# Optimization experiments

Measured on AMD Instinct MI355X. Metric: run time of the kernel, lower is better.

Reference implementation:

```python
import jax, jax.numpy as jnp
import numpy as np

EPS = 1e-5

def _layernorm(x, g, b):
    m = jnp.mean(x, axis=-1, keepdims=True)
    v = jnp.mean((x - m) ** 2, axis=-1, keepdims=True)
    return (x - m) * jax.lax.rsqrt(v + EPS) * g + b

def setup_inputs() -> dict:
    key = jax.random.key(0)
    ks = jax.random.split(key, 8)
    B, S, E, F = 32, 4096, 8, 512
    return {
        "x": jax.random.normal(ks[0], (B, S, E), dtype=jnp.float32),
        "W_in_attn": jax.random.normal(ks[1], (E, E), dtype=jnp.float32) * (1.0 / np.sqrt(E)),
        "theta_attn": jax.random.normal(ks[2], (E,), dtype=jnp.float32),
        "W_out": jax.random.normal(ks[3], (E, E), dtype=jnp.float32) * (1.0 / np.sqrt(E)),
        "theta_ffn": jax.random.normal(ks[4], (E,), dtype=jnp.float32),
        "W1": jax.random.normal(ks[5], (F, E), dtype=jnp.float32) * (1.0 / np.sqrt(E)),
        "b1": jnp.zeros((F,), dtype=jnp.float32),
        "W2": jax.random.normal(ks[6], (E, F), dtype=jnp.float32) * (1.0 / np.sqrt(F)),
        "b2": jnp.zeros((E,), dtype=jnp.float32),
        "ln1_g": jnp.ones((E,), dtype=jnp.float32),
        "ln1_b": jnp.zeros((E,), dtype=jnp.float32),
        "ln2_g": jnp.ones((E,), dtype=jnp.float32),
        "ln2_b": jnpp_zeros((E,)) if False else jnp.zeros((E,), dtype=jnp.float32),
    }

def reference(x, W_in_attn, theta_attn, W_out, theta_ffn, W1, b1, W2, b2,
              ln1_g, ln1_b, ln2_g, ln2_b):
    # --- quantum attention ---
    # per-wire circuit: RX(v_i) then trainable RX(theta_i) on |0>; <Z> = cos(v_i + theta_i)
    tv = jnp.einsum('bse,fe->bsf', x, W_in_attn)          # [B,S,8] input_proj (no bias)
    q_attn = jnp.cos(tv + theta_attn)                      # batched state-vector sim, closed form
    attn_out = jnp.einsum('bsf,ef->bse', q_attn, W_out)    # out_proj (no bias)
    # gate_residual=False, dropout inactive (eval)
    h = _layernorm(x + attn_out, ln1_g, ln1_b)
    # --- quantum FFN ---
    # per-wire circuit: RX(h_i) then trainable RY(theta_i); <Z> = cos(h_i) * cos(theta_i)
    q_ffn = jnp.cos(h) * jnp.cos(theta_ffn)               # [B,S,8]
    mid = jnp.einsum('bse,fe->bsf', q_ffn, W1) + b1        # linear1 -> [B,S,512]
    ffn_out = jnp.einsum('bsf,ef->bsf' if False else 'bsf,ef->bse', jax.nn.relu(mid), W2) + b2
    return _layernorm(h + ffn_out, ln2_g, ln2_b)
```

## Files before the change

### kernel.cpp

```cpp
#include <hip/hip_runtime.h>


typedef __attribute__((ext_vector_type(8)))  short short8;
typedef __attribute__((ext_vector_type(4)))  float f32x4;
typedef __attribute__((ext_vector_type(16))) float f32x16;
typedef __attribute__((ext_vector_type(4)))  int   int4v;

constexpr int E   = 8;
constexpr int F   = 512;
constexpr int TPB = 256;

static __device__ __forceinline__ int cvt_pk_bf16(float lo, float hi) {
    int r;
    asm("v_cvt_pk_bf16_f32 %0, %1, %2" : "=v"(r) : "v"(lo), "v"(hi));
    return r;
}

static __device__ __forceinline__ int hilo_bf16(float v) {
    unsigned u = __builtin_bit_cast(unsigned, v);
    float fh = __builtin_bit_cast(float, u & 0xFFFF0000u);
    return cvt_pk_bf16(fh, v - fh);
}

__global__ __launch_bounds__(512, 4) void qtb_kernel(
    const float* __restrict__ x,
    const float* __restrict__ Win,
    const float* __restrict__ th_attn,
    const float* __restrict__ Wout,
    const float* __restrict__ th_ffn,
    const float* __restrict__ W1,
    const float* __restrict__ b1,
    const float* __restrict__ W2,
    const float* __restrict__ b2,
    const float* __restrict__ g1, const float* __restrict__ bb1,
    const float* __restrict__ g2, const float* __restrict__ bb2,
    float* __restrict__ out, int ntok)
{
    __shared__ short8 wab[1024];
    __shared__ short8 w2p[512];
    __shared__ short8 attnA[64];
    __shared__ short8 woutp[64];

    const int tid  = threadIdx.x;
    const int lane = tid & 63;
    const int wv   = tid >> 6;
    const int t32  = lane & 31;
    const int hi   = lane >> 5;
    const int e8   = t32 & 7;

    {
        const f32x4* w1v = reinterpret_cast<const f32x4*>(W1 + tid * 8);
        f32x4 a = w1v[0], b = w1v[1];
        int4v rw1 = { cvt_pk_bf16(a[0], a[1]), cvt_pk_bf16(a[2], a[3]),
                      cvt_pk_bf16(b[0], b[1]), cvt_pk_bf16(b[2], b[3]) };
        wab[((tid >> 5) << 6) + (tid & 31)] = __builtin_bit_cast(short8, rw1);
        int4v rb1 = { hilo_bf16(b1[tid]), 0, 0, 0 };
        wab[((tid >> 5) << 6) + 32 + (tid & 31)] = __builtin_bit_cast(short8, rb1);
        const int se = tid & 7, sh = (tid >> 3) & 1, sm = (tid >> 4) & 1, sc = tid >> 5;
        const int f0 = sc * 32 + sm * 16 + sh * 4;
        const float* wp = W2 + se * F + f0;
        f32x4 p = *reinterpret_cast<const f32x4*>(wp);
        f32x4 q = *reinterpret_cast<const f32x4*>(wp + 8);
        int4v rw2 = { cvt_pk_bf16(p[0], p[1]), cvt_pk_bf16(p[2], p[3]),
                      cvt_pk_bf16(q[0], q[1]), cvt_pk_bf16(q[2], q[3]) };
        w2p[tid] = __builtin_bit_cast(short8, rw2);

        if (tid < 64) {
            const int tt = tid & 31;
            int4v ra = { 0, 0, 0, 0 };
            if (tt < 8) {
                if (tid < 32) {
                    const f32x4* wiv = reinterpret_cast<const f32x4*>(Win + tt * 8);
                    f32x4 wa = wiv[0], wb = wiv[1];
                    ra = int4v{ cvt_pk_bf16(wa[0], wa[1]), cvt_pk_bf16(wa[2], wa[3]),
                                cvt_pk_bf16(wb[0], wb[1]), cvt_pk_bf16(wb[2], wb[3]) };
                } else {
                    ra = int4v{ hilo_bf16(th_attn[tt]), 0, 0, 0 };
                }
            }
            attnA[tid] = __builtin_bit_cast(short8, ra);
        } else if (tid < 128) {
            const int l = tid - 64, tt = l & 31, hh = l >> 5;
            int4v ro = { 0, 0, 0, 0 };
            if (tt < 8) {
                const float* wo = Wout + tt * 8 + hh * 4;
                ro.x = cvt_pk_bf16(wo[0], wo[1]);
                ro.y = cvt_pk_bf16(wo[2], wo[3]);
            }
            woutp[l] = __builtin_bit_cast(short8, ro);
        }
    }
    __syncthreads();

    const int T = blockIdx.x * TPB + wv * 32 + t32;
    const bool valid = (T < ntok);
    const int ONE2 = 0x3F803F80;
    const f32x16 z16 = {};

    f32x4 x0 = {0.f,0.f,0.f,0.f}, x1 = {0.f,0.f,0.f,0.f};
    if (valid) {
        const f32x4* xv = reinterpret_cast<const f32x4*>(x + (size_t)T * E);
        x0 = xv[0]; x1 = xv[1];
    }

    int4v bx = hi ? int4v{ ONE2, 0, 0, 0 }
                  : int4v{ cvt_pk_bf16(x0[0], x0[1]), cvt_pk_bf16(x0[2], x0[3]),
                           cvt_pk_bf16(x1[0], x1[1]), cvt_pk_bf16(x1[2], x1[3]) };
    short8 aA = attnA[lane];
    f32x16 d1 = __builtin_amdgcn_mfma_f32_32x32x16_bf16(
        aA, __builtin_bit_cast(short8, bx), z16, 0, 0, 0);

    float qv0 = __cosf(d1[0]), qv1 = __cosf(d1[1]);
    float qv2 = __cosf(d1[2]), qv3 = __cosf(d1[3]);

    int q01 = cvt_pk_bf16(qv0, qv1), q23 = cvt_pk_bf16(qv2, qv3);
    int4v bq2 = { q01, q23, q01, q23 };
    short8 aO = woutp[lane];
    f32x16 c2 = z16;
    c2[0] = hi ? x1[0] : x0[0];
    c2[1] = hi ? x1[1] : x0[1];
    c2[2] = hi ? x1[2] : x0[2];
    c2[3] = hi ? x1[3] : x0[3];
    f32x16 d2 = __builtin_amdgcn_mfma_f32_32x32x16_bf16(
        aO, __builtin_bit_cast(short8, bq2), c2, 0, 0, 0);

    float po0 = d2[0], po1 = d2[1], po2 = d2[2], po3 = d2[3];
    float qo0 = __shfl_xor(po0, 32), qo1 = __shfl_xor(po1, 32);
    float qo2 = __shfl_xor(po2, 32), qo3 = __shfl_xor(po3, 32);
    float hv[8];
    hv[0] = hi ? qo0 : po0;  hv[1] = hi ? qo1 : po1;
    hv[2] = hi ? qo2 : po2;  hv[3] = hi ? qo3 : po3;
    hv[4] = hi ? po0 : qo0;  hv[5] = hi ? po1 : qo1;
    hv[6] = hi ? po2 : qo2;  hv[7] = hi ? po3 : qo3;

    float h[8];
    {
        float m = 0.f;
        #pragma unroll
        for (int e = 0; e < 8; ++e) m += hv[e];
        m *= 0.125f;
        float v = 0.f;
        #pragma unroll
        for (int e = 0; e < 8; ++e) { float d = hv[e] - m; v += d * d; }
        v *= 0.125f;
        float rs = rsqrtf(v + 1e-5f);
        #pragma unroll
        for (int e = 0; e < 8; ++e) h[e] = (hv[e] - m) * rs * g1[e] + bb1[e];
    }

    float qf[8];
    #pragma unroll
    for (int e = 0; e < 8; ++e) qf[e] = __cosf(h[e]) * __cosf(th_ffn[e]);
    int4v bqf = hi ? int4v{ ONE2, 0, 0, 0 }
                   : int4v{ cvt_pk_bf16(qf[0], qf[1]), cvt_pk_bf16(qf[2], qf[3]),
                            cvt_pk_bf16(qf[4], qf[5]), cvt_pk_bf16(qf[6], qf[7]) };
    short8 bqfs = __builtin_bit_cast(short8, bqf);

    f32x16 acc = z16;
    #pragma unroll 4
    for (int c = 0; c < 16; ++c) {
        short8 aW = wab[(c << 6) + lane];
        f32x16 m1 = __builtin_amdgcn_mfma_f32_32x32x16_bf16(aW, bqfs, z16, 0, 0, 0);
        float r0  = fmaxf(m1[0], 0.f),  r1  = fmaxf(m1[1], 0.f);
        float r2  = fmaxf(m1[2], 0.f),  r3  = fmaxf(m1[3], 0.f);
        float r4  = fmaxf(m1[4], 0.f),  r5  = fmaxf(m1[5], 0.f);
        float r6  = fmaxf(m1[6], 0.f),  r7  = fmaxf(m1[7], 0.f);
        float r8  = fmaxf(m1[8], 0.f),  r9  = fmaxf(m1[9], 0.f);
        float r10 = fmaxf(m1[10], 0.f), r11 = fmaxf(m1[11], 0.f);
        float r12 = fmaxf(m1[12], 0.f), r13 = fmaxf(m1[13], 0.f);
        float r14 = fmaxf(m1[14], 0.f), r15 = fmaxf(m1[15], 0.f);
        int4v pA = { cvt_pk_bf16(r0,  r1),  cvt_pk_bf16(r2,  r3),
                     cvt_pk_bf16(r4,  r5),  cvt_pk_bf16(r6,  r7) };
        int4v pB = { cvt_pk_bf16(r8,  r9),  cvt_pk_bf16(r10, r11),
                     cvt_pk_bf16(r12, r13), cvt_pk_bf16(r14, r15) };
        short8 wa0 = w2p[(c << 5) + (hi << 3) + e8];
        short8 wa1 = w2p[(c << 5) + 16 + (hi << 3) + e8];
        acc = __builtin_amdgcn_mfma_f32_32x32x16_bf16(
            wa0, __builtin_bit_cast(short8, pA), acc, 0, 0, 0);
        acc = __builtin_amdgcn_mfma_f32_32x32x16_bf16(
            wa1, __builtin_bit_cast(short8, pB), acc, 0, 0, 0);
    }

    float h0 = hi ? h[4] : h[0], h1 = hi ? h[5] : h[1];
    float h2 = hi ? h[6] : h[2], h3 = hi ? h[7] : h[3];
    float bz0 = hi ? b2[4] : b2[0], bz1 = hi ? b2[5] : b2[1];
    float bz2 = hi ? b2[6] : b2[2], bz3 = hi ? b2[7] : b2[3];
    float oh0 = h0 + acc[0] + bz0, oh1 = h1 + acc[1] + bz1;
    float oh2 = h2 + acc[2] + bz2, oh3 = h3 + acc[3] + bz3;
    float sw0 = __shfl_xor(oh0, 32), sw1 = __shfl_xor(oh1, 32);
    float sw2 = __shfl_xor(oh2, 32), sw3 = __shfl_xor(oh3, 32);
    float o[8];
    o[0] = hi ? sw0 : oh0;  o[1] = hi ? sw1 : oh1;
    o[2] = hi ? sw2 : oh2;  o[3] = hi ? sw3 : oh3;
    o[4] = hi ? oh0 : sw0;  o[5] = hi ? oh1 : sw1;
    o[6] = hi ? oh2 : sw2;  o[7] = hi ? oh3 : sw3;

    float m2 = 0.f;
    #pragma unroll
    for (int e = 0; e < 8; ++e) m2 += o[e];
    m2 *= 0.125f;
    float v2 = 0.f;
    #pragma unroll
    for (int e = 0; e < 8; ++e) { float d = o[e] - m2; v2 += d * d; }
    v2 *= 0.125f;
    float rs2 = rsqrtf(v2 + 1e-5f);
    float n[8];
    #pragma unroll
    for (int e = 0; e < 8; ++e) n[e] = (o[e] - m2) * rs2 * g2[e] + bb2[e];

    if (valid) {
        f32x4 st;
        st[0] = hi ? n[4] : n[0];  st[1] = hi ? n[5] : n[1];
        st[2] = hi ? n[6] : n[2];  st[3] = hi ? n[7] : n[3];
        *reinterpret_cast<f32x4*>(out + (size_t)T * E + hi * 4) = st;
    }
}

extern "C" void kernel_launch(void* const* d_in, const int* in_sizes, int n_in,
                              void* d_out, int out_size, void* d_ws, size_t ws_size,
                              hipStream_t stream) {
    const float* x       = (const float*)d_in[0];
    const float* Win     = (const float*)d_in[1];
    const float* th_attn = (const float*)d_in[2];
    const float* Wout    = (const float*)d_in[3];
    const float* th_ffn  = (const float*)d_in[4];
    const float* W1      = (const float*)d_in[5];
    const float* b1      = (const float*)d_in[6];
    const float* W2      = (const float*)d_in[7];
    const float* b2      = (const float*)d_in[8];
    const float* g1      = (const float*)d_in[9];
    const float* bb1     = (const float*)d_in[10];
    const float* g2      = (const float*)d_in[11];
    const float* bb2     = (const float*)d_in[12];
    float* out = (float*)d_out;
    (void)d_ws; (void)ws_size;

    const int ntok = in_sizes[0] / E;
    const int blocks = (ntok + TPB - 1) / TPB;
    qtb_kernel<<<blocks, 512, 0, stream>>>(x, Win, th_attn, Wout, th_ffn,
                                           W1, b1, W2, b2, g1, bb1, g2, bb2,
                                           out, ntok);
}
```

Baseline: 15.53 us.

## Compute layernorms on half-rows with partial-sum shuffles and split MFMA accumulators

```diff
diff --git a/kernel.cpp b/kernel.cpp
--- a/kernel.cpp
+++ b/kernel.cpp
@@ -40,6 +40,7 @@
     __shared__ short8 w2p[512];
     __shared__ short8 attnA[64];
     __shared__ short8 woutp[64];
+    __shared__ __align__(16) float cth_lds[8];
 
     const int tid  = threadIdx.x;
     const int lane = tid & 63;
@@ -64,6 +65,8 @@
         int4v rw2 = { cvt_pk_bf16(p[0], p[1]), cvt_pk_bf16(p[2], p[3]),
                       cvt_pk_bf16(q[0], q[1]), cvt_pk_bf16(q[2], q[3]) };
         w2p[tid] = __builtin_bit_cast(short8, rw2);
+
+        if (tid < 8) cth_lds[tid] = __cosf(th_ffn[tid]);
 
         if (tid < 64) {
             const int tt = tid & 31;
@@ -124,43 +127,35 @@
     f32x16 d2 = __builtin_amdgcn_mfma_f32_32x32x16_bf16(
         aO, __builtin_bit_cast(short8, bq2), c2, 0, 0, 0);
 
-    float po0 = d2[0], po1 = d2[1], po2 = d2[2], po3 = d2[3];
-    float qo0 = __shfl_xor(po0, 32), qo1 = __shfl_xor(po1, 32);
-    float qo2 = __shfl_xor(po2, 32), qo3 = __shfl_xor(po3, 32);
-    float hv[8];
-    hv[0] = hi ? qo0 : po0;  hv[1] = hi ? qo1 : po1;
-    hv[2] = hi ? qo2 : po2;  hv[3] = hi ? qo3 : po3;
-    hv[4] = hi ? po0 : qo0;  hv[5] = hi ? po1 : qo1;
-    hv[6] = hi ? po2 : qo2;  hv[7] = hi ? po3 : qo3;
-
-    float h[8];
-    {
-        float m = 0.f;
-        #pragma unroll
-        for (int e = 0; e < 8; ++e) m += hv[e];
-        m *= 0.125f;
-        float v = 0.f;
-        #pragma unroll
-        for (int e = 0; e < 8; ++e) { float d = hv[e] - m; v += d * d; }
-        v *= 0.125f;
-        float rs = rsqrtf(v + 1e-5f);
-        #pragma unroll
-        for (int e = 0; e < 8; ++e) h[e] = (hv[e] - m) * rs * g1[e] + bb1[e];
-    }
-
-    float qf[8];
-    #pragma unroll
-    for (int e = 0; e < 8; ++e) qf[e] = __cosf(h[e]) * __cosf(th_ffn[e]);
+    float s0 = d2[0], s1 = d2[1], s2 = d2[2], s3 = d2[3];
+    float ps = s0 + s1 + s2 + s3;
+    float pq = s0*s0 + s1*s1 + s2*s2 + s3*s3;
+    float mn = (ps + __shfl_xor(ps, 32)) * 0.125f;
+    float vr = (pq + __shfl_xor(pq, 32)) * 0.125f - mn * mn;
+    float rs = rsqrtf(vr + 1e-5f);
+    float hn[4];
+    hn[0] = (s0 - mn) * rs * g1[4 * hi + 0] + bb1[4 * hi + 0];
+    hn[1] = (s1 - mn) * rs * g1[4 * hi + 1] + bb1[4 * hi + 1];
+    hn[2] = (s2 - mn) * rs * g1[4 * hi + 2] + bb1[4 * hi + 2];
+    hn[3] = (s3 - mn) * rs * g1[4 * hi + 3] + bb1[4 * hi + 3];
+
+    f32x4 cthv = *reinterpret_cast<const f32x4*>(&cth_lds[hi * 4]);
+    float qf0 = __cosf(hn[0]) * cthv[0];
+    float qf1 = __cosf(hn[1]) * cthv[1];
+    float qf2 = __cosf(hn[2]) * cthv[2];
+    float qf3 = __cosf(hn[3]) * cthv[3];
+    int qa = cvt_pk_bf16(qf0, qf1), qb = cvt_pk_bf16(qf2, qf3);
+    int oqa = __shfl_xor(qa, 32), oqb = __shfl_xor(qb, 32);
     int4v bqf = hi ? int4v{ ONE2, 0, 0, 0 }
-                   : int4v{ cvt_pk_bf16(qf[0], qf[1]), cvt_pk_bf16(qf[2], qf[3]),
-                            cvt_pk_bf16(qf[4], qf[5]), cvt_pk_bf16(qf[6], qf[7]) };
+                   : int4v{ qa, qb, oqa, oqb };
     short8 bqfs = __builtin_bit_cast(short8, bqf);
 
-    f32x16 acc = z16;
+    f32x16 accA = z16, accB = z16;
     #pragma unroll 4
     for (int c = 0; c < 16; ++c) {
         short8 aW = wab[(c << 6) + lane];
-        f32x16 m1 = __builtin_amdgcn_mfma_f32_32x32x16_bf16(aW, bqfs, z16, 0, 0, 0);
+        f32x16 m1 = __builtin_amdgcn_mfma_f32_32x32x16_bf16(
+            aW, bqfs, z16, 0, 0, 0);
         float r0  = fmaxf(m1[0], 0.f),  r1  = fmaxf(m1[1], 0.f);
         float r2  = fmaxf(m1[2], 0.f),  r3  = fmaxf(m1[3], 0.f);
         float r4  = fmaxf(m1[4], 0.f),  r5  = fmaxf(m1[5], 0.f);
@@ -175,43 +170,27 @@
                      cvt_pk_bf16(r12, r13), cvt_pk_bf16(r14, r15) };
         short8 wa0 = w2p[(c << 5) + (hi << 3) + e8];
         short8 wa1 = w2p[(c << 5) + 16 + (hi << 3) + e8];
-        acc = __builtin_amdgcn_mfma_f32_32x32x16_bf16(
-            wa0, __builtin_bit_cast(short8, pA), acc, 0, 0, 0);
-        acc = __builtin_amdgcn_mfma_f32_32x32x16_bf16(
-            wa1, __builtin_bit_cast(short8, pB), acc, 0, 0, 0);
-    }
-
-    float h0 = hi ? h[4] : h[0], h1 = hi ? h[5] : h[1];
-    float h2 = hi ? h[6] : h[2], h3 = hi ? h[7] : h[3];
-    float bz0 = hi ? b2[4] : b2[0], bz1 = hi ? b2[5] : b2[1];
-    float bz2 = hi ? b2[6] : b2[2], bz3 = hi ? b2[7] : b2[3];
-    float oh0 = h0 + acc[0] + bz0, oh1 = h1 + acc[1] + bz1;
-    float oh2 = h2 + acc[2] + bz2, oh3 = h3 + acc[3] + bz3;
-    float sw0 = __shfl_xor(oh0, 32), sw1 = __shfl_xor(oh1, 32);
-    float sw2 = __shfl_xor(oh2, 32), sw3 = __shfl_xor(oh3, 32);
-    float o[8];
-    o[0] = hi ? sw0 : oh0;  o[1] = hi ? sw1 : oh1;
-    o[2] = hi ? sw2 : oh2;  o[3] = hi ? sw3 : oh3;
-    o[4] = hi ? oh0 : sw0;  o[5] = hi ? oh1 : sw1;
-    o[6] = hi ? oh2 : sw2;  o[7] = hi ? oh3 : sw3;
-
-    float m2 = 0.f;
+        accA = __builtin_amdgcn_mfma_f32_32x32x16_bf16(
+            wa0, __builtin_bit_cast(short8, pA), accA, 0, 0, 0);
+        accB = __builtin_amdgcn_mfma_f32_32x32x16_bf16(
+            wa1, __builtin_bit_cast(short8, pB), accB, 0, 0, 0);
+    }
+
+    float oi[4];
     #pragma unroll
-    for (int e = 0; e < 8; ++e) m2 += o[e];
-    m2 *= 0.125f;
-    float v2 = 0.f;
-    #pragma unroll
-    for (int e = 0; e < 8; ++e) { float d = o[e] - m2; v2 += d * d; }
-    v2 *= 0.125f;
+    for (int i = 0; i < 4; ++i)
+        oi[i] = hn[i] + accA[i] + accB[i] + b2[4 * hi + i];
+    float ps2 = oi[0] + oi[1] + oi[2] + oi[3];
+    float pq2 = oi[0]*oi[0] + oi[1]*oi[1] + oi[2]*oi[2] + oi[3]*oi[3];
+    float m2 = (ps2 + __shfl_xor(ps2, 32)) * 0.125f;
+    float v2 = (pq2 + __shfl_xor(pq2, 32)) * 0.125f - m2 * m2;
     float rs2 = rsqrtf(v2 + 1e-5f);
-    float n[8];
-    #pragma unroll
-    for (int e = 0; e < 8; ++e) n[e] = (o[e] - m2) * rs2 * g2[e] + bb2[e];
 
     if (valid) {
         f32x4 st;
-        st[0] = hi ? n[4] : n[0];  st[1] = hi ? n[5] : n[1];
-        st[2] = hi ? n[6] : n[2];  st[3] = hi ? n[7] : n[3];
+        #pragma unroll
+        for (int i = 0; i < 4; ++i)
+            st[i] = (oi[i] - m2) * rs2 * g2[4 * hi + i] + bb2[4 * hi + i];
         *reinterpret_cast<f32x4*>(out + (size_t)T * E + hi * 4) = st;
     }
 }
```

Result: no change. 15.43 us (-0.7%).
